# Optimization experiments

Measured on AMD Instinct MI355X. Metric: run time of the kernel, lower is better.

The kernel has to match this reference:

```python
import jax, jax.numpy as jnp
import numpy as np

B, DIM, RES = 32, 384, 28
KEY_DIM, HEADS, RATIO = 32, 8, 4
D = RATIO * KEY_DIM            # 128 value dim per head
DH = D * HEADS                 # 1024
NHKD = KEY_DIM * HEADS         # 256
H_QKV = DH + 2 * NHKD          # 1536
N = RES * RES                  # 784 tokens
EPS = 1e-5
SCALE = KEY_DIM ** -0.5


def _bias_idxs():
    pts = [(i, j) for i in range(RES) for j in range(RES)]
    offs, idxs = {}, []
    for p1 in pts:
        for p2 in pts:
            o = (abs(p1[0] - p2[0]), abs(p1[1] - p2[1]))
            if o not in offs:
                offs[o] = len(offs)
            idxs.append(offs[o])
    return np.asarray(idxs, np.int32).reshape(N, N), len(offs)


def hardswish(x):
    return x * jnp.clip(x + 3.0, 0.0, 6.0) * (1.0 / 6.0)


def bn_eval(x, g, b, m, v):
    # inference-mode BatchNorm2d over channel axis 1
    s = (g / jnp.sqrt(v + EPS))[None, :, None, None]
    return (x - m[None, :, None, None]) * s + b[None, :, None, None]


def setup_inputs() -> dict:
    key = jax.random.key(0)
    ks = jax.random.split(key, 12)
    idxs, n_off = _bias_idxs()
    return {
        "x": jax.random.normal(ks[0], (B, DIM, RES, RES), jnp.float32),
        "qkv_w": jax.random.normal(ks[1], (H_QKV, DIM), jnp.float32) * 0.02,
        "qkv_g": jax.random.uniform(ks[2], (H_QKV,), jnp.float32, 0.5, 1.5),
        "qkv_b": jax.random.normal(ks[3], (H_QKV,), jnp.float32) * 0.1,
        "qkv_m": jax.random.normal(ks[4], (H_QKV,), jnp.float32) * 0.1,
        "qkv_v": jax.random.uniform(ks[5], (H_QKV,), jnp.float32, 0.5, 1.5),
        "attn_biases": jax.random.normal(ks[6], (HEADS, n_off), jnp.float32) * 0.02,
        "proj_w": jax.random.normal(ks[7], (DIM, DH), jnp.float32) * 0.02,
        "proj_g": jax.random.uniform(ks[8], (DIM,), jnp.float32, 0.5, 1.5),
        "proj_b": jax.random.normal(ks[9], (DIM,), jnp.float32) * 0.1,
        "proj_m": jax.random.normal(ks[10], (DIM,), jnp.float32) * 0.1,
        "proj_v": jax.random.uniform(ks[11], (DIM,), jnp.float32, 0.5, 1.5),
        "bias_idxs": jnp.asarray(idxs),
    }


def reference(x, qkv_w, qkv_g, qkv_b, qkv_m, qkv_v, attn_biases,
              proj_w, proj_g, proj_b, proj_m, proj_v, bias_idxs):
    Bb, C, Hh, Ww = x.shape
    n = Hh * Ww
    # qkv: 1x1 conv + BN + hardswish
    y = jnp.einsum('bchw,oc->bohw', x, qkv_w)
    y = hardswish(bn_eval(y, qkv_g, qkv_b, qkv_m, qkv_v))
    y = y.reshape(Bb, HEADS, H_QKV // HEADS, n)
    q, k, v = jnp.split(y, [KEY_DIM, 2 * KEY_DIM], axis=2)  # [B,h,kd,N] x2, [B,h,d,N]
    bias = attn_biases[:, bias_idxs]                         # [heads, N, N]
    attn = jnp.einsum('bhkn,bhkm->bhnm', q, k) * SCALE + bias[None]
    attn = jax.nn.softmax(attn, axis=-1)
    out = jnp.einsum('bhdm,bhnm->bhdn', v, attn)             # v @ attn^T
    out = out.reshape(Bb, DH, Hh, Ww)
    # proj: hardswish -> 1x1 conv + BN + hardswish
    out = hardswish(out)
    out = jnp.einsum('bchw,oc->bohw', out, proj_w)
    out = hardswish(bn_eval(out, proj_g, proj_b, proj_m, proj_v))
    return out
```

## Files before the change

### kernel.cpp

```cpp
#include <hip/hip_runtime.h>
#include <cstdint>

constexpr int BATCH = 32;
constexpr int DIMC  = 384;
constexpr int NTOK  = 784;
constexpr int KD    = 32;
constexpr int DV    = 128;
constexpr int PERH  = 192;
constexpr int HQKV  = 1536;
constexpr int DHTOT = 1024;
constexpr int NMC   = 25;
constexpr int VPB   = NMC * 8 * 512;
constexpr float BNEPS  = 1e-5f;
constexpr float LOG2E  = 1.4426950408889634f;
constexpr float QSCL2  = 0.17677669529663687f * LOG2E;

#define DEVFN static __device__ __forceinline__

using f16x8 = __attribute__((ext_vector_type(8))) _Float16;
using f32x4 = __attribute__((ext_vector_type(4))) float;

DEVFN float hswish(float x) {
  float t = fminf(fmaxf(x + 3.0f, 0.0f), 6.0f);
  return x * t * (1.0f / 6.0f);
}
DEVFN uint16_t f2h(float f) { return __builtin_bit_cast(uint16_t, (_Float16)f); }
DEVFN float h2f(uint16_t u) { return (float)__builtin_bit_cast(_Float16, u); }
DEVFN uint32_t pk2h(float a, float b) {
  return __builtin_bit_cast(uint32_t, __builtin_amdgcn_cvt_pkrtz(a, b));
}

DEVFN void gload16(const void* g, void* l) {
  __builtin_amdgcn_global_load_lds(
      (const __attribute__((address_space(1))) void*)g,
      (__attribute__((address_space(3))) void*)l, 16, 0, 0);
}

__global__ __launch_bounds__(256) void convert_w(
    const float* __restrict__ qw, const float* __restrict__ pw,
    uint16_t* __restrict__ qwh, uint16_t* __restrict__ pwh)
{
  constexpr int QW4 = (HQKV * DIMC) / 4;
  constexpr int PW4 = (DIMC * DHTOT) / 4;
  int idx = blockIdx.x * 256 + threadIdx.x;
  if (idx < QW4) {
    float4 v = reinterpret_cast<const float4*>(qw)[idx];
    uint2 p;
    p.x = pk2h(v.x, v.y);
    p.y = pk2h(v.z, v.w);
    reinterpret_cast<uint2*>(qwh)[idx] = p;
  } else if (idx < QW4 + PW4) {
    int i2 = idx - QW4;
    float4 v = reinterpret_cast<const float4*>(pw)[i2];
    uint2 p;
    p.x = pk2h(v.x, v.y);
    p.y = pk2h(v.z, v.w);
    reinterpret_cast<uint2*>(pwh)[i2] = p;
  }
}

__global__ __launch_bounds__(256) void bias_build(
    const float* __restrict__ biases, uint16_t* __restrict__ biasH)
{
  const int n = blockIdx.x, h = blockIdx.y;
  const int t = threadIdx.x;
  if (t >= 196) return;
  const int m0 = 4*t;
  const int ri = (n * 2341) >> 16;
  const int rj = n - ri*28;
  const float* bh_ = biases + (size_t)h * NTOK;
  uint16_t o[4];
  #pragma unroll
  for (int r = 0; r < 4; ++r) {
    int m  = m0 + r;
    int im = (m * 2341) >> 16;
    int jm = m - im*28;
    int di = ri - im; di = di < 0 ? -di : di;
    int dj = rj - jm; dj = dj < 0 ? -dj : dj;
    o[r] = f2h(bh_[di*28 + dj] * LOG2E);
  }
  uint2 p;
  p.x = (uint32_t)o[0] | ((uint32_t)o[1] << 16);
  p.y = (uint32_t)o[2] | ((uint32_t)o[3] << 16);
  *reinterpret_cast<uint2*>(biasH + ((size_t)h*NTOK + n)*NTOK + m0) = p;
}

__global__ __launch_bounds__(256) void transpose_x(
    const float* __restrict__ x, uint16_t* __restrict__ xT)
{
  const int b = blockIdx.z, n0 = blockIdx.x * 32, c0 = blockIdx.y * 32;
  __shared__ float t[32][33];
  const int tx = threadIdx.x & 31, ty = threadIdx.x >> 5;
  const float* xb = x + (size_t)b * DIMC * NTOK;
  #pragma unroll
  for (int k = 0; k < 4; ++k) {
    int c = c0 + ty + 8*k;
    int n = n0 + tx;
    t[ty + 8*k][tx] = (n < NTOK) ? xb[(size_t)c * NTOK + n] : 0.f;
  }
  __syncthreads();
  uint16_t* xTb = xT + (size_t)b * NTOK * DIMC;
  #pragma unroll
  for (int k = 0; k < 4; ++k) {
    int n = n0 + ty + 8*k;
    if (n < NTOK) xTb[(size_t)n * DIMC + c0 + tx] = f2h(t[tx][ty + 8*k]);
  }
}

__global__ __launch_bounds__(256) void qkv_gemm(
    const uint16_t* __restrict__ wh, const uint16_t* __restrict__ xT,
    const float* __restrict__ gw, const float* __restrict__ bw,
    const float* __restrict__ mw, const float* __restrict__ vw,
    uint16_t* __restrict__ qb, uint16_t* __restrict__ kb, uint16_t* __restrict__ vb)
{
  const int b  = blockIdx.z;
  const int m0 = blockIdx.y * 128;
  const int n0 = blockIdx.x * 64;
  __shared__ __align__(16) uint16_t As[2][128*64];
  __shared__ __align__(16) uint16_t Bs[2][64*64];

  const int tid = threadIdx.x;
  const int w = tid >> 6, l = tid & 63, lg = l >> 4, ln = l & 15;
  const int wr = w >> 1, wc = w & 1;
  const int wbase = tid & 192;
  const uint16_t* xb = xT + (size_t)b * NTOK * DIMC;

  f32x4 acc[4][2];
  #pragma unroll
  for (int mi = 0; mi < 4; ++mi)
    #pragma unroll
    for (int ni = 0; ni < 2; ++ni) acc[mi][ni] = (f32x4){0.f,0.f,0.f,0.f};

  auto stage = [&](int buf, int k0) {
    #pragma unroll
    for (int j = 0; j < 4; ++j) {
      int s = j*256 + tid;
      int row = s >> 3, sl = s & 7;
      int srck = k0 + 8 * (sl ^ (row & 7));
      gload16(wh + (size_t)(m0 + row) * DIMC + srck,
              &As[buf][(j*256 + wbase) * 8]);
    }
    #pragma unroll
    for (int j = 0; j < 2; ++j) {
      int s = j*256 + tid;
      int row = s >> 3, sl = s & 7;
      int nrow = n0 + row; if (nrow > NTOK-1) nrow = NTOK-1;
      int srck = k0 + 8 * (sl ^ (row & 7));
      gload16(xb + (size_t)nrow * DIMC + srck,
              &Bs[buf][(j*256 + wbase) * 8]);
    }
  };

  stage(0, 0);
  int cur = 0;
  for (int k0 = 0; k0 < DIMC; k0 += 64) {
    __syncthreads();
    if (k0 + 64 < DIMC) stage(cur ^ 1, k0 + 64);
    #pragma unroll
    for (int kk = 0; kk < 2; ++kk) {
      f16x8 af[4], bf[2];
      #pragma unroll
      for (int mi = 0; mi < 4; ++mi) {
        int row = 64*wr + 16*mi + ln;
        int slot = (4*kk + lg) ^ (row & 7);
        af[mi] = *reinterpret_cast<const f16x8*>(&As[cur][row*64 + slot*8]);
      }
      #pragma unroll
      for (int ni = 0; ni < 2; ++ni) {
        int row = 32*wc + 16*ni + ln;
        int slot = (4*kk + lg) ^ (row & 7);
        bf[ni] = *reinterpret_cast<const f16x8*>(&Bs[cur][row*64 + slot*8]);
      }
      #pragma unroll
      for (int mi = 0; mi < 4; ++mi)
        #pragma unroll
        for (int ni = 0; ni < 2; ++ni)
          acc[mi][ni] = __builtin_amdgcn_mfma_f32_16x16x32_f16(
              af[mi], bf[ni], acc[mi][ni], 0, 0, 0);
    }
    cur ^= 1;
  }

  #pragma unroll
  for (int mi = 0; mi < 4; ++mi) {
    const int ob = m0 + 64*wr + 16*mi;
    const int h  = ob / PERH;
    const int r0 = ob - h * PERH;
    const int bh = b*8 + h;
    float sc[4], sh[4];
    #pragma unroll
    for (int r = 0; r < 4; ++r) {
      int o = ob + 4*lg + r;
      float s = gw[o] * rsqrtf(vw[o] + BNEPS);
      sc[r] = s; sh[r] = bw[o] - mw[o]*s;
    }
    #pragma unroll
    for (int ni = 0; ni < 2; ++ni) {
      int n = n0 + 32*wc + 16*ni + ln;
      if (n >= NTOK) continue;
      float v4[4];
      #pragma unroll
      for (int r = 0; r < 4; ++r) v4[r] = hswish(acc[mi][ni][r]*sc[r] + sh[r]);
      if (r0 < 2*KD) {
        if (r0 < KD) {
          #pragma unroll
          for (int r = 0; r < 4; ++r) v4[r] *= QSCL2;
        }
        uint16_t* base = (r0 < KD) ? qb : kb;
        int dd = (r0 & 16) + 4*lg;
        uint2 p;
        p.x = pk2h(v4[0], v4[1]);
        p.y = pk2h(v4[2], v4[3]);
        *reinterpret_cast<uint2*>(base + ((size_t)bh*NTOK + n)*KD + dd) = p;
      } else {
        const int dv0 = r0 - 2*KD;
        const int mc = n >> 5, mm = n & 31;
        const int lgv = mm >> 3, jj = mm & 7;
        uint16_t* vblk = vb + (size_t)bh*VPB + ((size_t)mc*8)*512 + lgv*128 + jj;
        #pragma unroll
        for (int r = 0; r < 4; ++r) {
          int dv = dv0 + 4*lg + r;
          int dt = dv >> 4, lnv = dv & 15;
          vblk[(size_t)dt*512 + lnv*8] = f2h(v4[r]);
        }
      }
    }
  }
}

__global__ __launch_bounds__(256) void attn_kernel(
    const uint16_t* __restrict__ Qb, const uint16_t* __restrict__ Kb,
    const uint16_t* __restrict__ Vb, const uint16_t* __restrict__ biasH,
    uint16_t* __restrict__ a2T)
{
  const int bh = blockIdx.x;
  const int b_ = bh >> 3;
  const int h  = bh & 7;

  __shared__ __align__(16) uint16_t plds[4][2][16][72];

  const int tid = threadIdx.x;
  const int w   = tid >> 6;
  const int l   = tid & 63;
  const int lg  = l >> 4;
  const int ln  = l & 15;

  const int tile = blockIdx.y * 4 + w;
  if (tile >= 25) return;
  const int n0 = tile * 32;
  const int nA = n0 + ln;
  int nBr = n0 + 16 + ln;
  const int nB = (nBr < NTOK) ? nBr : (NTOK-1);

  const uint16_t* Kbase = Kb + (size_t)bh * NTOK * KD;
  const uint16_t* Vbase = Vb + (size_t)bh * VPB;
  const uint16_t* browA = biasH + ((size_t)h * NTOK + nA) * NTOK;
  const uint16_t* browB = biasH + ((size_t)h * NTOK + nB) * NTOK;

  const f16x8 qfA = *reinterpret_cast<const f16x8*>(
      Qb + ((size_t)bh*NTOK + nA)*KD + 8*lg);
  const f16x8 qfB = *reinterpret_cast<const f16x8*>(
      Qb + ((size_t)bh*NTOK + nB)*KD + 8*lg);

  float MA = -1e30f, LA = 0.f, MB = -1e30f, LB = 0.f;
  f32x4 accA[8], accB[8];
  #pragma unroll
  for (int dt = 0; dt < 8; ++dt) {
    accA[dt] = (f32x4){0.f,0.f,0.f,0.f};
    accB[dt] = (f32x4){0.f,0.f,0.f,0.f};
  }

  for (int mb = 0; mb < NTOK; mb += 64) {
    const int rem   = (NTOK - mb) >> 4;
    const int ntile = rem < 4 ? rem : 4;
    const int mc0   = mb >> 5;

    float pA[16], pB[16];
    #pragma unroll
    for (int i = 0; i < 16; ++i) { pA[i] = -1e30f; pB[i] = -1e30f; }

    #pragma unroll
    for (int t = 0; t < 4; ++t) {
      if (t < ntile) {
        f16x8 kf = *reinterpret_cast<const f16x8*>(
            Kbase + (size_t)(mb + 16*t + ln)*KD + 8*lg);
        uint2 ba = *reinterpret_cast<const uint2*>(browA + mb + 16*t + 4*lg);
        uint2 bb = *reinterpret_cast<const uint2*>(browB + mb + 16*t + 4*lg);
        f32x4 cA, cB;
        cA[0] = h2f((uint16_t)(ba.x & 0xffffu)); cA[1] = h2f((uint16_t)(ba.x >> 16));
        cA[2] = h2f((uint16_t)(ba.y & 0xffffu)); cA[3] = h2f((uint16_t)(ba.y >> 16));
        cB[0] = h2f((uint16_t)(bb.x & 0xffffu)); cB[1] = h2f((uint16_t)(bb.x >> 16));
        cB[2] = h2f((uint16_t)(bb.y & 0xffffu)); cB[3] = h2f((uint16_t)(bb.y >> 16));
        f32x4 sA = __builtin_amdgcn_mfma_f32_16x16x32_f16(kf, qfA, cA, 0, 0, 0);
        f32x4 sB = __builtin_amdgcn_mfma_f32_16x16x32_f16(kf, qfB, cB, 0, 0, 0);
        #pragma unroll
        for (int r = 0; r < 4; ++r) { pA[4*t+r] = sA[r]; pB[4*t+r] = sB[r]; }
      }
    }

    f16x8 vf0[8];
    #pragma unroll
    for (int dt = 0; dt < 8; ++dt)
      vf0[dt] = *reinterpret_cast<const f16x8*>(
          Vbase + ((size_t)mc0*8 + dt)*512 + l*8);

    float mxA = pA[0], mxB = pB[0];
    #pragma unroll
    for (int i = 1; i < 16; ++i) { mxA = fmaxf(mxA, pA[i]); mxB = fmaxf(mxB, pB[i]); }
    mxA = fmaxf(mxA, __shfl_xor(mxA, 16)); mxA = fmaxf(mxA, __shfl_xor(mxA, 32));
    mxB = fmaxf(mxB, __shfl_xor(mxB, 16)); mxB = fmaxf(mxB, __shfl_xor(mxB, 32));

    float MnA = fmaxf(MA, mxA), MnB = fmaxf(MB, mxB);
    float alA = exp2f(MA - MnA), alB = exp2f(MB - MnB);
    float sumA = 0.f, sumB = 0.f;
    #pragma unroll
    for (int i = 0; i < 16; ++i) {
      pA[i] = exp2f(pA[i] - MnA); sumA += pA[i];
      pB[i] = exp2f(pB[i] - MnB); sumB += pB[i];
    }
    sumA += __shfl_xor(sumA, 16); sumA += __shfl_xor(sumA, 32);
    sumB += __shfl_xor(sumB, 16); sumB += __shfl_xor(sumB, 32);
    LA = LA * alA + sumA; MA = MnA;
    LB = LB * alB + sumB; MB = MnB;

    float alA4[4], alB4[4];
    #pragma unroll
    for (int r = 0; r < 4; ++r) {
      alA4[r] = __shfl(alA, 20*lg + r);
      alB4[r] = __shfl(alB, 20*lg + r);
    }
    #pragma unroll
    for (int dt = 0; dt < 8; ++dt) {
      #pragma unroll
      for (int r = 0; r < 4; ++r) { accA[dt][r] *= alA4[r]; accB[dt][r] *= alB4[r]; }
    }

    #pragma unroll
    for (int t = 0; t < 4; ++t) {
      uint2 ka, kb2;
      ka.x  = pk2h(pA[4*t+0], pA[4*t+1]);
      ka.y  = pk2h(pA[4*t+2], pA[4*t+3]);
      kb2.x = pk2h(pB[4*t+0], pB[4*t+1]);
      kb2.y = pk2h(pB[4*t+2], pB[4*t+3]);
      *reinterpret_cast<uint2*>(&plds[w][0][ln][16*t + 4*lg]) = ka;
      *reinterpret_cast<uint2*>(&plds[w][1][ln][16*t + 4*lg]) = kb2;
    }

    {
      f16x8 pfA = *reinterpret_cast<const f16x8*>(&plds[w][0][ln][8*lg]);
      f16x8 pfB = *reinterpret_cast<const f16x8*>(&plds[w][1][ln][8*lg]);
      __builtin_amdgcn_s_setprio(1);
      #pragma unroll
      for (int dt = 0; dt < 8; ++dt) {
        accA[dt] = __builtin_amdgcn_mfma_f32_16x16x32_f16(pfA, vf0[dt], accA[dt], 0, 0, 0);
        accB[dt] = __builtin_amdgcn_mfma_f32_16x16x32_f16(pfB, vf0[dt], accB[dt], 0, 0, 0);
      }
      __builtin_amdgcn_s_setprio(0);
    }

    if (mb + 32 < NTOK) {
      f16x8 pfA = *reinterpret_cast<const f16x8*>(&plds[w][0][ln][32 + 8*lg]);
      f16x8 pfB = *reinterpret_cast<const f16x8*>(&plds[w][1][ln][32 + 8*lg]);
      f16x8 vf1[8];
      #pragma unroll
      for (int dt = 0; dt < 8; ++dt)
        vf1[dt] = *reinterpret_cast<const f16x8*>(
            Vbase + ((size_t)(mc0+1)*8 + dt)*512 + l*8);
      __builtin_amdgcn_s_setprio(1);
      #pragma unroll
      for (int dt = 0; dt < 8; ++dt) {
        accA[dt] = __builtin_amdgcn_mfma_f32_16x16x32_f16(pfA, vf1[dt], accA[dt], 0, 0, 0);
        accB[dt] = __builtin_amdgcn_mfma_f32_16x16x32_f16(pfB, vf1[dt], accB[dt], 0, 0, 0);
      }
      __builtin_amdgcn_s_setprio(0);
    }
  }

  float liA = 1.0f / LA, liB = 1.0f / LB;
  float liA4[4], liB4[4];
  #pragma unroll
  for (int r = 0; r < 4; ++r) {
    liA4[r] = __shfl(liA, 20*lg + r);
    liB4[r] = __shfl(liB, 20*lg + r);
  }
  #pragma unroll
  for (int r = 0; r < 4; ++r) {
    int rowA = n0 + 4*lg + r;
    #pragma unroll
    for (int dt = 0; dt < 8; ++dt)
      a2T[((size_t)b_*NTOK + rowA)*DHTOT + h*DV + 16*dt + ln] =
          f2h(hswish(accA[dt][r] * liA4[r]));
    int rowB = n0 + 16 + 4*lg + r;
    if (rowB < NTOK) {
      #pragma unroll
      for (int dt = 0; dt < 8; ++dt)
        a2T[((size_t)b_*NTOK + rowB)*DHTOT + h*DV + 16*dt + ln] =
            f2h(hswish(accB[dt][r] * liB4[r]));
    }
  }
}

__global__ __launch_bounds__(256) void proj_gemm(
    const uint16_t* __restrict__ wh, const uint16_t* __restrict__ a2T,
    const float* __restrict__ gw, const float* __restrict__ bw,
    const float* __restrict__ mw, const float* __restrict__ vw,
    float* __restrict__ out)
{
  const int b  = blockIdx.z;
  const int m0 = blockIdx.y * 128;
  const int n0 = blockIdx.x * 64;
  __shared__ __align__(16) uint16_t As[2][128*64];
  __shared__ __align__(16) uint16_t Bs[2][64*64];

  const int tid = threadIdx.x;
  const int w = tid >> 6, l = tid & 63, lg = l >> 4, ln = l & 15;
  const int wr = w >> 1, wc = w & 1;
  const int wbase = tid & 192;
  const uint16_t* ab = a2T + (size_t)b * NTOK * DHTOT;

  f32x4 acc[4][2];
  #pragma unroll
  for (int mi = 0; mi < 4; ++mi)
    #pragma unroll
    for (int ni = 0; ni < 2; ++ni) acc[mi][ni] = (f32x4){0.f,0.f,0.f,0.f};

  auto stage = [&](int buf, int k0) {
    #pragma unroll
    for (int j = 0; j < 4; ++j) {
      int s = j*256 + tid;
      int row = s >> 3, sl = s & 7;
      int srck = k0 + 8 * (sl ^ (row & 7));
      gload16(wh + (size_t)(m0 + row) * DHTOT + srck,
              &As[buf][(j*256 + wbase) * 8]);
    }
    #pragma unroll
    for (int j = 0; j < 2; ++j) {
      int s = j*256 + tid;
      int row = s >> 3, sl = s & 7;
      int nrow = n0 + row; if (nrow > NTOK-1) nrow = NTOK-1;
      int srck = k0 + 8 * (sl ^ (row & 7));
      gload16(ab + (size_t)nrow * DHTOT + srck,
              &Bs[buf][(j*256 + wbase) * 8]);
    }
  };

  stage(0, 0);
  int cur = 0;
  for (int k0 = 0; k0 < DHTOT; k0 += 64) {
    __syncthreads();
    if (k0 + 64 < DHTOT) stage(cur ^ 1, k0 + 64);
    #pragma unroll
    for (int kk = 0; kk < 2; ++kk) {
      f16x8 af[4], bf[2];
      #pragma unroll
      for (int mi = 0; mi < 4; ++mi) {
        int row = 64*wr + 16*mi + ln;
        int slot = (4*kk + lg) ^ (row & 7);
        af[mi] = *reinterpret_cast<const f16x8*>(&As[cur][row*64 + slot*8]);
      }
      #pragma unroll
      for (int ni = 0; ni < 2; ++ni) {
        int row = 32*wc + 16*ni + ln;
        int slot = (4*kk + lg) ^ (row & 7);
        bf[ni] = *reinterpret_cast<const f16x8*>(&Bs[cur][row*64 + slot*8]);
      }
      #pragma unroll
      for (int mi = 0; mi < 4; ++mi)
        #pragma unroll
        for (int ni = 0; ni < 2; ++ni)
          acc[mi][ni] = __builtin_amdgcn_mfma_f32_16x16x32_f16(
              af[mi], bf[ni], acc[mi][ni], 0, 0, 0);
    }
    cur ^= 1;
  }

  #pragma unroll
  for (int mi = 0; mi < 4; ++mi) {
    float sc[4], sh[4];
    #pragma unroll
    for (int r = 0; r < 4; ++r) {
      int o = m0 + 64*wr + 16*mi + 4*lg + r;
      float s = gw[o] * rsqrtf(vw[o] + BNEPS);
      sc[r] = s; sh[r] = bw[o] - mw[o]*s;
    }
    #pragma unroll
    for (int ni = 0; ni < 2; ++ni) {
      int n = n0 + 32*wc + 16*ni + ln;
      if (n >= NTOK) continue;
      #pragma unroll
      for (int r = 0; r < 4; ++r) {
        int o = m0 + 64*wr + 16*mi + 4*lg + r;
        out[((size_t)b*DIMC + o)*NTOK + n] = hswish(acc[mi][ni][r]*sc[r] + sh[r]);
      }
    }
  }
}

extern "C" void kernel_launch(void* const* d_in, const int* in_sizes, int n_in,
                              void* d_out, int out_size, void* d_ws, size_t ws_size,
                              hipStream_t stream)
{
  const float* x  = (const float*)d_in[0];
  const float* qw = (const float*)d_in[1];
  const float* qg = (const float*)d_in[2];
  const float* qb_ = (const float*)d_in[3];
  const float* qm = (const float*)d_in[4];
  const float* qv = (const float*)d_in[5];
  const float* ab = (const float*)d_in[6];
  const float* pw = (const float*)d_in[7];
  const float* pg = (const float*)d_in[8];
  const float* pb = (const float*)d_in[9];
  const float* pm = (const float*)d_in[10];
  const float* pv = (const float*)d_in[11];
  float* out = (float*)d_out;

  uint16_t* qwh   = (uint16_t*)d_ws;
  uint16_t* pwh   = qwh + (size_t)HQKV * DIMC;
  uint16_t* biasH = pwh + (size_t)DIMC * DHTOT;
  uint16_t* dyn   = biasH + (size_t)8 * NTOK * NTOK;
  const size_t fixed_bytes =
      ((size_t)HQKV*DIMC + (size_t)DIMC*DHTOT + (size_t)8*NTOK*NTOK) * 2;

  const size_t XT_B = (size_t)NTOK * DIMC;
  const size_t QK_B = (size_t)8 * NTOK * KD;
  const size_t V_B  = (size_t)8 * VPB;
  const size_t A2_B = (size_t)NTOK * DHTOT;
  const size_t PER_B = XT_B + 2*QK_B + V_B + A2_B;

  size_t avail = (ws_size > fixed_bytes) ? (ws_size - fixed_bytes) : 0;
  int nb = (int)(avail / (PER_B * 2));
  if (nb > BATCH) nb = BATCH;
  if (nb < 1) nb = 1;

  uint16_t* xTb  = dyn;
  uint16_t* qbuf = xTb  + (size_t)nb * XT_B;
  uint16_t* kbuf = qbuf + (size_t)nb * QK_B;
  uint16_t* vbuf = kbuf + (size_t)nb * QK_B;
  uint16_t* a2   = vbuf + (size_t)nb * V_B;

  convert_w<<<960, 256, 0, stream>>>(qw, pw, qwh, pwh);
  bias_build<<<dim3(NTOK, 8), 256, 0, stream>>>(ab, biasH);

  for (int b0 = 0; b0 < BATCH; b0 += nb) {
    int cb = BATCH - b0; if (cb > nb) cb = nb;
    const float* xb = x + (size_t)b0 * DIMC * NTOK;
    float* ob = out + (size_t)b0 * DIMC * NTOK;

    transpose_x<<<dim3(25, 12, cb), 256, 0, stream>>>(xb, xTb);
    qkv_gemm<<<dim3(13, 12, cb), 256, 0, stream>>>(qwh, xTb, qg, qb_, qm, qv,
                                                   qbuf, kbuf, vbuf);
    attn_kernel<<<dim3(cb * 8, 7), 256, 0, stream>>>(qbuf, kbuf, vbuf, biasH, a2);
    proj_gemm<<<dim3(13, 3, cb), 256, 0, stream>>>(pwh, a2, pg, pb, pm, pv, ob);
  }
}
```

Baseline: 311.2 us.

## Prefetch next K/bias tiles, skip unchanged-max rescale, tree-reduce softmax

Software-pipelines the attention loop so the K fragments and the two bias rows for the next 64-key block are loaded while the current block is processed, hiding global-load latency. The accumulator and denominator rescale is skipped wave-wide whenever no row's running max increased. The max and sum reductions become balanced trees to shorten dependency chains. The prefetch raises register pressure, since it holds 4 K vectors plus 8 bias words live across the loop, and it adds a divergent branch.

New measurement: 350.7 us. 1.13x slower.

```diff
diff --git a/kernel.cpp b/kernel.cpp
--- a/kernel.cpp
+++ b/kernel.cpp
@@ -270,6 +270,20 @@
     accB[dt] = (f32x4){0.f,0.f,0.f,0.f};
   }
 
+  f16x8 kf[4];
+  uint2  ba[4], bb[4];
+  auto loadKB = [&](int mbase) {
+    #pragma unroll
+    for (int t = 0; t < 4; ++t) {
+      int mrow = mbase + 16*t + ln; if (mrow > NTOK-1) mrow = NTOK-1;
+      kf[t] = *reinterpret_cast<const f16x8*>(Kbase + (size_t)mrow*KD + 8*lg);
+      int mo = mbase + 16*t + 4*lg; if (mo > NTOK-4) mo = NTOK-4;
+      ba[t] = *reinterpret_cast<const uint2*>(browA + mo);
+      bb[t] = *reinterpret_cast<const uint2*>(browB + mo);
+    }
+  };
+  loadKB(0);
+
   for (int mb = 0; mb < NTOK; mb += 64) {
     const int rem   = (NTOK - mb) >> 4;
     const int ntile = rem < 4 ? rem : 4;
@@ -282,21 +296,19 @@
     #pragma unroll
     for (int t = 0; t < 4; ++t) {
       if (t < ntile) {
-        f16x8 kf = *reinterpret_cast<const f16x8*>(
-            Kbase + (size_t)(mb + 16*t + ln)*KD + 8*lg);
-        uint2 ba = *reinterpret_cast<const uint2*>(browA + mb + 16*t + 4*lg);
-        uint2 bb = *reinterpret_cast<const uint2*>(browB + mb + 16*t + 4*lg);
         f32x4 cA, cB;
-        cA[0] = h2f((uint16_t)(ba.x & 0xffffu)); cA[1] = h2f((uint16_t)(ba.x >> 16));
-        cA[2] = h2f((uint16_t)(ba.y & 0xffffu)); cA[3] = h2f((uint16_t)(ba.y >> 16));
-        cB[0] = h2f((uint16_t)(bb.x & 0xffffu)); cB[1] = h2f((uint16_t)(bb.x >> 16));
-        cB[2] = h2f((uint16_t)(bb.y & 0xffffu)); cB[3] = h2f((uint16_t)(bb.y >> 16));
-        f32x4 sA = __builtin_amdgcn_mfma_f32_16x16x32_f16(kf, qfA, cA, 0, 0, 0);
-        f32x4 sB = __builtin_amdgcn_mfma_f32_16x16x32_f16(kf, qfB, cB, 0, 0, 0);
+        cA[0] = h2f((uint16_t)(ba[t].x & 0xffffu)); cA[1] = h2f((uint16_t)(ba[t].x >> 16));
+        cA[2] = h2f((uint16_t)(ba[t].y & 0xffffu)); cA[3] = h2f((uint16_t)(ba[t].y >> 16));
+        cB[0] = h2f((uint16_t)(bb[t].x & 0xffffu)); cB[1] = h2f((uint16_t)(bb[t].x >> 16));
+        cB[2] = h2f((uint16_t)(bb[t].y & 0xffffu)); cB[3] = h2f((uint16_t)(bb[t].y >> 16));
+        f32x4 sA = __builtin_amdgcn_mfma_f32_16x16x32_f16(kf[t], qfA, cA, 0, 0, 0);
+        f32x4 sB = __builtin_amdgcn_mfma_f32_16x16x32_f16(kf[t], qfB, cB, 0, 0, 0);
         #pragma unroll
         for (int r = 0; r < 4; ++r) { pA[4*t+r] = sA[r]; pB[4*t+r] = sB[r]; }
       }
     }
+
+    if (mb + 64 < NTOK) loadKB(mb + 64);
 
     f16x8 vf0[8];
     #pragma unroll
@@ -304,36 +316,62 @@
       vf0[dt] = *reinterpret_cast<const f16x8*>(
           Vbase + ((size_t)mc0*8 + dt)*512 + l*8);
 
-    float mxA = pA[0], mxB = pB[0];
-    #pragma unroll
-    for (int i = 1; i < 16; ++i) { mxA = fmaxf(mxA, pA[i]); mxB = fmaxf(mxB, pB[i]); }
-    mxA = fmaxf(mxA, __shfl_xor(mxA, 16)); mxA = fmaxf(mxA, __shfl_xor(mxA, 32));
-    mxB = fmaxf(mxB, __shfl_xor(mxB, 16)); mxB = fmaxf(mxB, __shfl_xor(mxB, 32));
+    float mA01, mB01;
+    {
+      float a0 = fmaxf(pA[0], pA[1]),  a1 = fmaxf(pA[2], pA[3]);
+      float a2 = fmaxf(pA[4], pA[5]),  a3 = fmaxf(pA[6], pA[7]);
+      float a4 = fmaxf(pA[8], pA[9]),  a5 = fmaxf(pA[10], pA[11]);
+      float a6 = fmaxf(pA[12], pA[13]), a7 = fmaxf(pA[14], pA[15]);
+      mA01 = fmaxf(fmaxf(fmaxf(a0,a1), fmaxf(a2,a3)), fmaxf(fmaxf(a4,a5), fmaxf(a6,a7)));
+      float b0 = fmaxf(pB[0], pB[1]),  b1 = fmaxf(pB[2], pB[3]);
+      float b2 = fmaxf(pB[4], pB[5]),  b3 = fmaxf(pB[6], pB[7]);
+      float b4 = fmaxf(pB[8], pB[9]),  b5 = fmaxf(pB[10], pB[11]);
+      float b6 = fmaxf(pB[12], pB[13]), b7 = fmaxf(pB[14], pB[15]);
+      mB01 = fmaxf(fmaxf(fmaxf(b0,b1), fmaxf(b2,b3)), fmaxf(fmaxf(b4,b5), fmaxf(b6,b7)));
+    }
+    float mxA = fmaxf(mA01, __shfl_xor(mA01, 16)); mxA = fmaxf(mxA, __shfl_xor(mxA, 32));
+    float mxB = fmaxf(mB01, __shfl_xor(mB01, 16)); mxB = fmaxf(mxB, __shfl_xor(mxB, 32));
 
     float MnA = fmaxf(MA, mxA), MnB = fmaxf(MB, mxB);
-    float alA = exp2f(MA - MnA), alB = exp2f(MB - MnB);
-    float sumA = 0.f, sumB = 0.f;
-    #pragma unroll
-    for (int i = 0; i < 16; ++i) {
-      pA[i] = exp2f(pA[i] - MnA); sumA += pA[i];
-      pB[i] = exp2f(pB[i] - MnB); sumB += pB[i];
+
+    if (!__all((mxA <= MA) & (mxB <= MB))) {
+      float alA = exp2f(MA - MnA), alB = exp2f(MB - MnB);
+      LA *= alA; LB *= alB;
+      float alA4[4], alB4[4];
+      #pragma unroll
+      for (int r = 0; r < 4; ++r) {
+        alA4[r] = __shfl(alA, 20*lg + r);
+        alB4[r] = __shfl(alB, 20*lg + r);
+      }
+      #pragma unroll
+      for (int dt = 0; dt < 8; ++dt) {
+        #pragma unroll
+        for (int r = 0; r < 4; ++r) { accA[dt][r] *= alA4[r]; accB[dt][r] *= alB4[r]; }
+      }
+    }
+    MA = MnA; MB = MnB;
+
+    float sumA, sumB;
+    {
+      #pragma unroll
+      for (int i = 0; i < 16; ++i) {
+        pA[i] = exp2f(pA[i] - MnA);
+        pB[i] = exp2f(pB[i] - MnB);
+      }
+      float s0 = (pA[0]+pA[1]) + (pA[2]+pA[3]);
+      float s1 = (pA[4]+pA[5]) + (pA[6]+pA[7]);
+      float s2 = (pA[8]+pA[9]) + (pA[10]+pA[11]);
+      float s3 = (pA[12]+pA[13]) + (pA[14]+pA[15]);
+      sumA = (s0+s1) + (s2+s3);
+      float t0 = (pB[0]+pB[1]) + (pB[2]+pB[3]);
+      float t1 = (pB[4]+pB[5]) + (pB[6]+pB[7]);
+      float t2 = (pB[8]+pB[9]) + (pB[10]+pB[11]);
+      float t3 = (pB[12]+pB[13]) + (pB[14]+pB[15]);
+      sumB = (t0+t1) + (t2+t3);
     }
     sumA += __shfl_xor(sumA, 16); sumA += __shfl_xor(sumA, 32);
     sumB += __shfl_xor(sumB, 16); sumB += __shfl_xor(sumB, 32);
-    LA = LA * alA + sumA; MA = MnA;
-    LB = LB * alB + sumB; MB = MnB;
-
-    float alA4[4], alB4[4];
-    #pragma unroll
-    for (int r = 0; r < 4; ++r) {
-      alA4[r] = __shfl(alA, 20*lg + r);
-      alB4[r] = __shfl(alB, 20*lg + r);
-    }
-    #pragma unroll
-    for (int dt = 0; dt < 8; ++dt) {
-      #pragma unroll
-      for (int r = 0; r < 4; ++r) { accA[dt][r] *= alA4[r]; accB[dt][r] *= alB4[r]; }
-    }
+    LA += sumA; LB += sumB;
 
     #pragma unroll
     for (int t = 0; t < 4; ++t) {
```
